# Optimization experiments

Hardware: AMD Instinct MI355X
Metric: run time of the kernel (lower is better)

## Reference

```python
import jax, jax.numpy as jnp
import numpy as np
from jax import lax

RADIUS = 0.3
NSAMPLE = 16
NPROP = 256
NHB = 12
NSC = 18
NCLS = 18
BNEPS = 1e-5


def setup_inputs() -> dict:
    key = jax.random.key(0)
    ks = jax.random.split(key, 10)
    B, K, C = 32, 2048, 256
    OUT = 2 + 3 + NHB * 2 + NSC * 4 + NCLS  # 119
    return {
        "xyz": jax.random.uniform(ks[0], (B, K, 3), jnp.float32),
        "features": jax.random.normal(ks[1], (B, C, K), jnp.float32),
        "sa_w1": jax.random.normal(ks[2], (256, C + 3), jnp.float32) * 0.05,
        "sa_w2": jax.random.normal(ks[3], (256, 256), jnp.float32) * 0.05,
        "sa_w3": jax.random.normal(ks[4], (256, 256), jnp.float32) * 0.05,
        "sa_gamma": jnp.ones((3, 256), jnp.float32),
        "sa_beta": jnp.zeros((3, 256), jnp.float32),
        "sa_mean": jnp.zeros((3, 256), jnp.float32),
        "sa_var": jnp.ones((3, 256), jnp.float32),
        "p_w1": jax.random.normal(ks[5], (256, 256), jnp.float32) * 0.05,
        "p_w2": jax.random.normal(ks[6], (256, 256), jnp.float32) * 0.05,
        "p_w3": jax.random.normal(ks[7], (OUT, 256), jnp.float32) * 0.05,
        "p_b3": jnp.zeros((OUT,), jnp.float32),
        "p_gamma": jnp.ones((2, 256), jnp.float32),
        "p_beta": jnp.zeros((2, 256), jnp.float32),
        "p_mean": jnp.zeros((2, 256), jnp.float32),
        "p_var": jnp.ones((2, 256), jnp.float32),
        "mean_size_arr": jax.random.uniform(ks[8], (NSC, 3), jnp.float32, 0.3, 1.5),
    }


def fps(xyz, npoint):
    # iterative furthest point sampling, starts at index 0 (matches CUDA kernel)
    B, K, _ = xyz.shape

    def body(carry, _):
        dist, far = carry
        centroid = jnp.take_along_axis(xyz, far[:, None, None], axis=1)  # (B,1,3)
        d = jnp.sum((xyz - centroid) ** 2, axis=-1)  # (B,K)
        dist = jnp.minimum(dist, d)
        nxt = jnp.argmax(dist, axis=-1).astype(jnp.int32)
        return (dist, nxt), far

    init = (jnp.full((B, K), 1e10, xyz.dtype), jnp.zeros((B,), jnp.int32))
    _, inds = lax.scan(body, init, None, length=npoint)
    return jnp.transpose(inds, (1, 0))  # (B, npoint)


def ball_query(new_xyz, xyz):
    # first NSAMPLE points (in original index order) within RADIUS; pad with first hit
    B, K, _ = xyz.shape
    d2 = jnp.sum((new_xyz[:, :, None, :] - xyz[:, None, :, :]) ** 2, axis=-1)  # (B,P,K)
    within = d2 < RADIUS * RADIUS
    cand = jnp.where(within, jnp.arange(K, dtype=jnp.int32)[None, None, :], K)
    cand = jnp.sort(cand, axis=-1)[..., :NSAMPLE]
    first = cand[..., :1]  # query point itself is always within radius
    return jnp.where(cand == K, first, cand)  # (B,P,NSAMPLE)


def box_corners(center_unnorm, size, angle):
    # flip_axis_to_camera: X right, Y down (-z_up), Z forward (y_up)
    cc = jnp.stack([center_unnorm[..., 0], center_unnorm[..., 2], -center_unnorm[..., 1]], axis=-1)
    c, s = jnp.cos(angle), jnp.sin(angle)
    zz, oo = jnp.zeros_like(angle), jnp.ones_like(angle)
    R = jnp.stack([c, zz, s, zz, oo, zz, -s, zz, c], axis=-1).reshape(angle.shape + (3, 3))
    sx = jnp.asarray([1, 1, -1, -1, 1, 1, -1, -1], jnp.float32)
    sy = jnp.asarray([1, 1, 1, 1, -1, -1, -1, -1], jnp.float32)
    sz = jnp.asarray([1, -1, -1, 1, 1, -1, -1, 1], jnp.float32)
    xc = size[..., 0:1] * sx * 0.5
    yc = size[..., 2:3] * sy * 0.5
    zc = size[..., 1:2] * sz * 0.5
    corners = jnp.stack([xc, yc, zc], axis=-2)  # (B,P,3,8)
    out = jnp.einsum('bpij,bpjk->bpik', R, corners) + cc[..., None]
    return jnp.transpose(out, (0, 1, 3, 2))  # (B,P,8,3)


def _forward(xyz, features, sa_w1, sa_w2, sa_w3, sa_gamma, sa_beta, sa_mean, sa_var,
             p_w1, p_w2, p_w3, p_b3, p_gamma, p_beta, p_mean, p_var, mean_size_arr):
    B, K, _ = xyz.shape
    inds = fps(xyz, NPROP)  # (B,P) vote_fps
    new_xyz = jnp.take_along_axis(xyz, inds[..., None], axis=1)  # (B,P,3)
    idx = ball_query(new_xyz, xyz)  # (B,P,S)
    flat = idx.reshape(B, -1)
    g_xyz = jnp.take_along_axis(xyz, flat[..., None], axis=1).reshape(B, NPROP, NSAMPLE, 3)
    g_xyz = (g_xyz - new_xyz[:, :, None, :]) / RADIUS  # normalize_xyz
    g_feat = jnp.take_along_axis(features, flat[:, None, :], axis=2).reshape(B, -1, NPROP, NSAMPLE)
    x = jnp.concatenate([jnp.transpose(g_xyz, (0, 3, 1, 2)), g_feat], axis=1)  # (B,3+C,P,S)
    for i, w in enumerate((sa_w1, sa_w2, sa_w3)):
        x = jnp.einsum('oc,bcps->bops', w, x)
        scale = (sa_gamma[i] / jnp.sqrt(sa_var[i] + BNEPS))[None, :, None, None]
        x = jax.nn.relu((x - sa_mean[i][None, :, None, None]) * scale + sa_beta[i][None, :, None, None])
    y = jnp.max(x, axis=-1)  # (B,256,P) max-pool over neighbors
    for i, w in enumerate((p_w1, p_w2)):
        y = jnp.einsum('oc,bcp->bop', w, y)
        scale = (p_gamma[i] / jnp.sqrt(p_var[i] + BNEPS))[None, :, None]
        y = jax.nn.relu((y - p_mean[i][None, :, None]) * scale + p_beta[i][None, :, None])
    net = jnp.einsum('oc,bcp->bop', p_w3, y) + p_b3[None, :, None]
    nt = jnp.transpose(net, (0, 2, 1))  # (B,P,119)
    obj = nt[..., 0:2]
    center = new_xyz + nt[..., 2:5]
    o = 5 + NHB * 2
    size_scores = nt[..., o:o + NSC]
    srn = nt[..., o + NSC:o + NSC * 4].reshape(B, NPROP, NSC, 3)
    sem = nt[..., o + NSC * 4:]
    size_res = srn * mean_size_arr[None, None]
    best = jnp.argmax(size_scores, axis=-1)
    pred_size = jnp.take_along_axis(size_res + mean_size_arr[None, None],
                                    best[..., None, None], axis=2)[:, :, 0, :]
    corners = box_corners(center, pred_size, jnp.zeros_like(center[..., 0]))
    sem_logits = jnp.concatenate(
        [sem, jnp.argmin(obj, axis=-1, keepdims=True).astype(nt.dtype) * 1e10], axis=-1)
    obj_prob = jax.nn.softmax(obj, axis=-1)[..., 1]
    sem_prob = jax.nn.softmax(sem, axis=-1)
    return obj, center, size_scores, size_res, pred_size, sem, corners, sem_logits, obj_prob, sem_prob


def reference(xyz, features, sa_w1, sa_w2, sa_w3, sa_gamma, sa_beta, sa_mean, sa_var,
              p_w1, p_w2, p_w3, p_b3, p_gamma, p_beta, p_mean, p_var, mean_size_arr):
    return _forward(xyz, features, sa_w1, sa_w2, sa_w3, sa_gamma, sa_beta, sa_mean, sa_var,
                    p_w1, p_w2, p_w3, p_b3, p_gamma, p_beta, p_mean, p_var, mean_size_arr)
```

## Files before the change

kernel.cpp:

```cpp
#include <hip/hip_runtime.h>
#include <math.h>

#define B_   32
#define K_   2048
#define C_   256
#define P_   256
#define S_   16
#define OUTC 119

#define OFF0 0
#define OFF1 16384
#define OFF2 40960
#define OFF3 188416
#define OFF4 630784
#define OFF5 655360
#define OFF6 802816
#define OFF7 999424
#define OFF8 1155072
#define OFF9 1163264

typedef _Float16 half8  __attribute__((ext_vector_type(8)));
typedef _Float16 half4h __attribute__((ext_vector_type(4)));
typedef float    f32x4  __attribute__((ext_vector_type(4)));
#define MFMA16 __builtin_amdgcn_mfma_f32_16x16x32_f16

#define XT 65

__device__ __forceinline__ float sqdist_rn(float ax, float ay, float az,
                                           float bx, float by, float bz) {
  float dx = __fsub_rn(ax, bx), dy = __fsub_rn(ay, by), dz = __fsub_rn(az, bz);
  return __fadd_rn(__fadd_rn(__fmul_rn(dx, dx), __fmul_rn(dy, dy)),
                   __fmul_rn(dz, dz));
}

__device__ __forceinline__ unsigned umax_(unsigned a, unsigned b) {
  return a > b ? a : b;
}
__device__ __forceinline__ unsigned umin_(unsigned a, unsigned b) {
  return a < b ? a : b;
}
__device__ __forceinline__ unsigned wave_red_umax(unsigned x) {
  x = umax_(x, (unsigned)__builtin_amdgcn_update_dpp(0, (int)x, 0x111, 0xf, 0xf, false));
  x = umax_(x, (unsigned)__builtin_amdgcn_update_dpp(0, (int)x, 0x112, 0xf, 0xf, false));
  x = umax_(x, (unsigned)__builtin_amdgcn_update_dpp(0, (int)x, 0x114, 0xf, 0xf, false));
  x = umax_(x, (unsigned)__builtin_amdgcn_update_dpp(0, (int)x, 0x118, 0xf, 0xf, false));
  x = umax_(x, (unsigned)__builtin_amdgcn_update_dpp(0, (int)x, 0x142, 0xf, 0xf, false));
  x = umax_(x, (unsigned)__builtin_amdgcn_update_dpp(0, (int)x, 0x143, 0xf, 0xf, false));
  return x;
}
__device__ __forceinline__ unsigned wave_red_umin(unsigned x) {
  x = umin_(x, (unsigned)__builtin_amdgcn_update_dpp(-1, (int)x, 0x111, 0xf, 0xf, false));
  x = umin_(x, (unsigned)__builtin_amdgcn_update_dpp(-1, (int)x, 0x112, 0xf, 0xf, false));
  x = umin_(x, (unsigned)__builtin_amdgcn_update_dpp(-1, (int)x, 0x114, 0xf, 0xf, false));
  x = umin_(x, (unsigned)__builtin_amdgcn_update_dpp(-1, (int)x, 0x118, 0xf, 0xf, false));
  x = umin_(x, (unsigned)__builtin_amdgcn_update_dpp(-1, (int)x, 0x142, 0xf, 0xf, false));
  x = umin_(x, (unsigned)__builtin_amdgcn_update_dpp(-1, (int)x, 0x143, 0xf, 0xf, false));
  return x;
}

__device__ __forceinline__ void wsplit_body(
    int r, int t, const float* __restrict__ w1, const float* __restrict__ w2,
    const float* __restrict__ w3, const float* __restrict__ pw1,
    const float* __restrict__ pw2, const float* __restrict__ gma,
    const float* __restrict__ var, const float* __restrict__ pg,
    const float* __restrict__ pv, _Float16* __restrict__ w1h,
    _Float16* __restrict__ w1l, _Float16* __restrict__ w2h,
    _Float16* __restrict__ w2l, _Float16* __restrict__ w3h,
    _Float16* __restrict__ w3l, _Float16* __restrict__ p1h,
    _Float16* __restrict__ p1l, _Float16* __restrict__ p2h,
    _Float16* __restrict__ p2l, float* __restrict__ bns) {
  if (r == 656) {
    for (int u = t; u < 768; u += 64) bns[u] = gma[u] / sqrtf(var[u] + 1e-5f);
    for (int u = t; u < 512; u += 64)
      bns[768 + u] = pg[u] / sqrtf(pv[u] + 1e-5f);
    return;
  }
  const float* src;
  _Float16 *dh, *dl;
  int ot, ks, nks, K, remap = 0;
  if (r < 144) {
    src = w1; dh = w1h; dl = w1l; ot = r / 9; ks = r % 9; nks = 9; K = 259;
    remap = 1;
  } else if (r < 272) {
    const int rr = r - 144;
    src = w2; dh = w2h; dl = w2l; ot = rr >> 3; ks = rr & 7; nks = 8; K = 256;
  } else if (r < 400) {
    const int rr = r - 272;
    src = w3; dh = w3h; dl = w3l; ot = rr >> 3; ks = rr & 7; nks = 8; K = 256;
  } else if (r < 528) {
    const int rr = r - 400;
    src = pw1; dh = p1h; dl = p1l; ot = rr >> 3; ks = rr & 7; nks = 8; K = 256;
  } else {
    const int rr = r - 528;
    src = pw2; dh = p2h; dl = p2l; ot = rr >> 3; ks = rr & 7; nks = 8; K = 256;
  }
  const int m = t & 15, q = t >> 4;
  const float* row = src + (ot * 16 + m) * K;
  half8 vh, vl;
#pragma unroll
  for (int j = 0; j < 8; j++) {
    const int c = ks * 32 + q * 8 + j;
    float v;
    if (remap) {
      v = (c < 3) ? row[c] : (c >= 8 && c < 264) ? row[c - 5] : 0.f;
    } else {
      v = (c < K) ? row[c] : 0.f;
    }
    const _Float16 hi = (_Float16)v;
    vh[j] = hi;
    vl[j] = (_Float16)(v - (float)hi);
  }
  const int base = ((ot * nks + ks) * 64 + t) * 8;
  *(half8*)&dh[base] = vh;
  *(half8*)&dl[base] = vl;
}

__global__ __launch_bounds__(256) void fused_pre_kernel(
    const float* __restrict__ xyz, float* __restrict__ new_xyz,
    const float* __restrict__ features, _Float16* __restrict__ ftH,
    _Float16* __restrict__ ftL,
    const float* __restrict__ w1, const float* __restrict__ w2,
    const float* __restrict__ w3, const float* __restrict__ pw1,
    const float* __restrict__ pw2, const float* __restrict__ gma,
    const float* __restrict__ var, const float* __restrict__ pg,
    const float* __restrict__ pv, _Float16* __restrict__ w1h,
    _Float16* __restrict__ w1l, _Float16* __restrict__ w2h,
    _Float16* __restrict__ w2l, _Float16* __restrict__ w3h,
    _Float16* __restrict__ w3l, _Float16* __restrict__ p1h,
    _Float16* __restrict__ p1l, _Float16* __restrict__ p2h,
    _Float16* __restrict__ p2l, float* __restrict__ bns) {
  __shared__ __align__(16) char smem_pre[32768];
  __shared__ uint2 redw[2][4];
  const int bid = blockIdx.x;

  if (bid >= 197) {
    const int idx = bid - 197;
    const int b = idx >> 7, rem = idx & 127;
    const int c0 = (rem >> 5) * 64, k0 = (rem & 31) * 64;
    float* tl = (float*)smem_pre;
    const int w = threadIdx.x >> 6, lane = threadIdx.x & 63;
    const float* fb = features + (size_t)b * C_ * K_;
#pragma unroll
    for (int r = 0; r < 16; r++) {
      const int cl = r * 4 + w;
      tl[cl * 65 + lane] = fb[(size_t)(c0 + cl) * K_ + k0 + lane];
    }
    __syncthreads();
#pragma unroll
    for (int r = 0; r < 16; r++) {
      const int kl = r * 4 + w;
      const float v = tl[lane * 65 + kl];
      const _Float16 hi = (_Float16)v;
      const size_t o = ((size_t)b * K_ + k0 + kl) * C_ + c0 + lane;
      ftH[o] = hi;
      ftL[o] = (_Float16)(v - (float)hi);
    }
    return;
  }

  if (bid >= 32) {
    const int sub = (bid - 32) * 4 + (threadIdx.x >> 6);
    if (sub < 657)
      wsplit_body(sub, threadIdx.x & 63, w1, w2, w3, pw1, pw2, gma, var, pg,
                  pv, w1h, w1l, w2h, w2l, w3h, w3l, p1h, p1l, p2h, p2l, bns);
    return;
  }

  const int b = bid, t = threadIdx.x;
  const int lane = t & 63, w = t >> 6;
  float4* pts = (float4*)smem_pre;
  const float* xb = xyz + b * K_ * 3;
  float px[8], py[8], pz[8], dist[8];
#pragma unroll
  for (int j = 0; j < 8; j++) {
    const int k = t + 256 * j;
    const float x = xb[3 * k + 0];
    const float yv = xb[3 * k + 1];
    const float z = xb[3 * k + 2];
    px[j] = x; py[j] = yv; pz[j] = z;
    dist[j] = 1e10f;
    pts[k] = make_float4(x, yv, z, 0.f);
  }
  __syncthreads();
  int far = 0;
  for (int i = 0; i < P_; i++) {
    const float4 c = pts[far];
    if (t == 0) {
      float* nx = new_xyz + (b * P_ + i) * 3;
      nx[0] = c.x; nx[1] = c.y; nx[2] = c.z;
    }
    float bv = -1.f;
    int bj = 0;
#pragma unroll
    for (int j = 0; j < 8; j++) {
      const float d = sqdist_rn(px[j], py[j], pz[j], c.x, c.y, c.z);
      dist[j] = fminf(dist[j], d);
      if (dist[j] > bv) { bv = dist[j]; bj = j; }
    }
    const unsigned bvb = __float_as_uint(bv);
    const unsigned gw = wave_red_umax(bvb);
    const unsigned gmaxw = (unsigned)__builtin_amdgcn_readlane((int)gw, 63);
    const unsigned kg = (unsigned)(bj * 256 + t);
    const unsigned key2 = (bvb == gmaxw) ? kg : 0xFFFFFFFFu;
    const unsigned kw = wave_red_umin(key2);
    if (lane == 63) redw[i & 1][w] = make_uint2(gmaxw, kw);
    __syncthreads();
    const uint2 r0 = redw[i & 1][0], r1 = redw[i & 1][1];
    const uint2 r2 = redw[i & 1][2], r3 = redw[i & 1][3];
    const unsigned g = umax_(umax_(r0.x, r1.x), umax_(r2.x, r3.x));
    unsigned fk = 0xFFFFFFFFu;
    if (r0.x == g) fk = umin_(fk, r0.y);
    if (r1.x == g) fk = umin_(fk, r1.y);
    if (r2.x == g) fk = umin_(fk, r2.y);
    if (r3.x == g) fk = umin_(fk, r3.y);
    far = (int)fk;
  }
}

__global__ __launch_bounds__(1024) void ballq_kernel(
    const float* __restrict__ xyz, const float* __restrict__ new_xyz,
    int* __restrict__ idxw) {
  const int blk = blockIdx.x;
  const int b = blk >> 4, pg = (blk & 15) * 16, t = threadIdx.x;
  __shared__ __align__(16) float4 pts[K_];
  const float* xb = xyz + b * K_ * 3;
#pragma unroll
  for (int j = 0; j < 2; j++) {
    const int k = t + 1024 * j;
    pts[k] = make_float4(xb[3 * k + 0], xb[3 * k + 1], xb[3 * k + 2], 0.f);
  }
  __syncthreads();
  const float r2 = (float)(0.3 * 0.3);
  const int w = t >> 6, lane = t & 63;
  const int p = pg + w;
  const float nx = new_xyz[(b * P_ + p) * 3 + 0];
  const float ny = new_xyz[(b * P_ + p) * 3 + 1];
  const float nz = new_xyz[(b * P_ + p) * 3 + 2];
  int* ob = idxw + (b * P_ + p) * S_;
  unsigned msk = 0u;
#pragma unroll
  for (int j = 0; j < 32; j++) {
    const float4 q = pts[j * 64 + lane];
    const float d2 = sqdist_rn(q.x, q.y, q.z, nx, ny, nz);
    msk |= (d2 < r2 ? 1u : 0u) << j;
  }
  int cnt = 0, first = -1;
  for (int j = 0; j < 32; j++) {
    const unsigned long long bal = __ballot((msk >> j) & 1u);
    if (bal != 0ull && first < 0) first = j * 64 + (__ffsll(bal) - 1);
    const int c = (int)__popcll(bal);
    if ((msk >> j) & 1u) {
      const int pos = cnt + (int)__popcll(bal & ((1ull << lane) - 1ull));
      if (pos < S_) ob[pos] = j * 64 + lane;
    }
    cnt += c;
    if (cnt >= S_) break;
  }
  if (cnt < S_ && lane < S_ - cnt) ob[cnt + lane] = first;
}

__global__ __launch_bounds__(512, 4) void sa_kernel(
    const float* __restrict__ xyz, const float* __restrict__ features,
    const _Float16* __restrict__ ftH, const _Float16* __restrict__ ftL,
    const int use_ft,
    const _Float16* __restrict__ w1h, const _Float16* __restrict__ w1l,
    const _Float16* __restrict__ w2h, const _Float16* __restrict__ w2l,
    const _Float16* __restrict__ w3h, const _Float16* __restrict__ w3l,
    const float* __restrict__ bns, const float* __restrict__ mu,
    const float* __restrict__ bta, const float* __restrict__ new_xyz,
    const int* __restrict__ idxw, float* __restrict__ y) {
  const int blk = blockIdx.x;
  const int b = blk >> 6, p0 = (blk & 63) * 4, t = threadIdx.x;
  __shared__ __align__(16) _Float16 Xh[36 * XT * 8];
  __shared__ __align__(16) _Float16 Xl[36 * XT * 8];
  __shared__ __align__(16) float red[4 * 256];
  __shared__ int k_sh[64];

  if (t < 64) k_sh[t] = idxw[(b * P_ + p0) * S_ + t];
  if (t < 192) {
    const int tile = 32 + t / 48, row = 16 + (t % 48);
    const half8 z8 = {};
    *(half8*)&Xh[(tile * XT + row) * 8] = z8;
    *(half8*)&Xl[(tile * XT + row) * 8] = z8;
  }
  __syncthreads();
  if (t < 64) {
    const int st = t >> 4, m = t & 15, k = k_sh[t];
    const float* xb = xyz + b * K_ * 3;
    const float* nx = new_xyz + (b * P_ + p0 + st) * 3;
    const int base = (st * XT + m) * 8;
#pragma unroll
    for (int c = 0; c < 3; c++) {
      const float v = (xb[3 * k + c] - nx[c]) / 0.3f;
      const _Float16 hi = (_Float16)v;
      Xh[base + c] = hi;
      Xl[base + c] = (_Float16)(v - (float)hi);
    }
#pragma unroll
    for (int j = 3; j < 8; j++) {
      Xh[base + j] = (_Float16)0.f;
      Xl[base + j] = (_Float16)0.f;
    }
  }
  if (use_ft) {
    for (int u = t; u < 2048; u += 512) {
      const int s = u >> 5, ch = u & 31;
      const int c = 8 + ch * 8;
      const int ks = c >> 5, q2 = (c >> 3) & 3;
      const int st = s >> 4, m = s & 15;
      const size_t ro = ((size_t)b * K_ + k_sh[s]) * C_ + ch * 8;
      const int row = (q2 * 16 + m) ^ (ks & 7);
      const int dst = ((ks * 4 + st) * XT + row) * 8;
      *(half8*)&Xh[dst] = *(const half8*)&ftH[ro];
      *(half8*)&Xl[dst] = *(const half8*)&ftL[ro];
    }
  } else {
    const int cl = t & 255, hf = t >> 8;
    const float* fb = features + (size_t)b * C_ * K_ + (size_t)cl * K_;
    const int c = 8 + cl;
    const int ks = c >> 5, q2 = (c >> 3) & 3, j = c & 7;
    const int s0 = hf * 32;
#pragma unroll 8
    for (int s = s0; s < s0 + 32; s++) {
      const float v = fb[k_sh[s]];
      const _Float16 hi = (_Float16)v;
      const int row = (q2 * 16 + (s & 15)) ^ (ks & 7);
      const int dst = ((ks * 4 + (s >> 4)) * XT + row) * 8 + j;
      Xh[dst] = hi;
      Xl[dst] = (_Float16)(v - (float)hi);
    }
  }

  const int lane = t & 63, w = t >> 6;
  const int m = lane & 15, q = lane >> 4;

  f32x4 acc[2][4];
  half8 rAh[2][2], rAl[2][2];
#pragma unroll
  for (int i = 0; i < 2; i++) {
    rAh[0][i] = *(const half8*)&w1h[(((2 * w + i) * 9 + 0) * 64 + lane) * 8];
    rAl[0][i] = *(const half8*)&w1l[(((2 * w + i) * 9 + 0) * 64 + lane) * 8];
    rAh[1][i] = *(const half8*)&w1h[(((2 * w + i) * 9 + 1) * 64 + lane) * 8];
    rAl[1][i] = *(const half8*)&w1l[(((2 * w + i) * 9 + 1) * 64 + lane) * 8];
  }
  __syncthreads();

#pragma unroll
  for (int l = 0; l < 3; l++) {
    const int nks = (l == 0) ? 9 : 8;
    const int base = (l == 0) ? 0 : (l == 1) ? 9 : 17;
#pragma unroll
    for (int i = 0; i < 2; i++)
#pragma unroll
      for (int s = 0; s < 4; s++) acc[i][s] = (f32x4){0.f, 0.f, 0.f, 0.f};
#pragma unroll
    for (int ks = 0; ks < nks; ks++) {
      const int par = (base + ks) & 1;
      half8 Ah[2], Al[2];
#pragma unroll
      for (int i = 0; i < 2; i++) { Ah[i] = rAh[par][i]; Al[i] = rAl[par][i]; }
      {
        int ln = l, kn = ks + 2;
        if (kn >= nks) { kn -= nks; ln = l + 1; }
        if (ln < 3) {
          const _Float16* Ph = (ln == 0) ? w1h : (ln == 1) ? w2h : w3h;
          const _Float16* Pl = (ln == 0) ? w1l : (ln == 1) ? w2l : w3l;
          const int nk2 = (ln == 0) ? 9 : 8;
#pragma unroll
          for (int i = 0; i < 2; i++) {
            const int off = (((2 * w + i) * nk2 + kn) * 64 + lane) * 8;
            rAh[par][i] = *(const half8*)&Ph[off];
            rAl[par][i] = *(const half8*)&Pl[off];
          }
        }
      }
      const int rsw = lane ^ (ks & 7);
#pragma unroll
      for (int s = 0; s < 4; s++) {
        const int tb = ((ks * 4 + s) * XT + rsw) * 8;
        const half8 Bh = *(const half8*)&Xh[tb];
        const half8 Bl = *(const half8*)&Xl[tb];
#pragma unroll
        for (int i = 0; i < 2; i++) {
          acc[i][s] = MFMA16(Ah[i], Bh, acc[i][s], 0, 0, 0);
          acc[i][s] = MFMA16(Ah[i], Bl, acc[i][s], 0, 0, 0);
          acc[i][s] = MFMA16(Al[i], Bh, acc[i][s], 0, 0, 0);
        }
      }
    }

    if (l < 2) {
      __syncthreads();
#pragma unroll
      for (int i = 0; i < 2; i++) {
        const int c0 = (2 * w + i) * 16 + q * 4;
        const int ks2 = c0 >> 5, q2 = (c0 >> 3) & 3, j0 = c0 & 7;
        const f32x4 sc4 = *(const f32x4*)&bns[l * 256 + c0];
        const f32x4 m4 = *(const f32x4*)&mu[l * 256 + c0];
        const f32x4 b4 = *(const f32x4*)&bta[l * 256 + c0];
        const int row = (q2 * 16 + m) ^ (ks2 & 7);
#pragma unroll
        for (int s = 0; s < 4; s++) {
          half4h vh, vl;
#pragma unroll
          for (int r = 0; r < 4; r++) {
            const float v = fmaxf((acc[i][s][r] - m4[r]) * sc4[r] + b4[r], 0.f);
            const _Float16 hi = (_Float16)v;
            vh[r] = hi;
            vl[r] = (_Float16)(v - (float)hi);
          }
          const int dst = ((ks2 * 4 + s) * XT + row) * 8 + j0;
          *(half4h*)&Xh[dst] = vh;
          *(half4h*)&Xl[dst] = vl;
        }
      }
      __syncthreads();
    } else {
#pragma unroll
      for (int i = 0; i < 2; i++)
#pragma unroll
        for (int s = 0; s < 4; s++)
#pragma unroll
          for (int r = 0; r < 4; r++) {
            float v = acc[i][s][r];
            v = fmaxf(v, __shfl_xor(v, 1));
            v = fmaxf(v, __shfl_xor(v, 2));
            v = fmaxf(v, __shfl_xor(v, 4));
            v = fmaxf(v, __shfl_xor(v, 8));
            acc[i][s][r] = v;
          }
      if (m == 0) {
#pragma unroll
        for (int i = 0; i < 2; i++) {
          const int ob = (2 * w + i) * 16 + q * 4;
#pragma unroll
          for (int s = 0; s < 4; s++) *(f32x4*)&red[s * 256 + ob] = acc[i][s];
        }
      }
      __syncthreads();
      for (int u = t; u < 1024; u += 512) {
        const int pl = u >> 8, col = u & 255;
        const float sc2 = bns[512 + col];
        const float mu2 = mu[512 + col], bt2 = bta[512 + col];
        const float raw = red[pl * 256 + col];
        y[(b * P_ + p0 + pl) * 256 + col] = fmaxf((raw - mu2) * sc2 + bt2, 0.f);
      }
    }
  }
}

__global__ __launch_bounds__(256, 2) void phead_kernel(
    const float* __restrict__ y, const _Float16* __restrict__ p1h,
    const _Float16* __restrict__ p1l, const _Float16* __restrict__ p2h,
    const _Float16* __restrict__ p2l, const float* __restrict__ pw3,
    const float* __restrict__ pb3, const float* __restrict__ bns,
    const float* __restrict__ pm, const float* __restrict__ pb,
    const float* __restrict__ new_xyz, const float* __restrict__ msa,
    float* __restrict__ out) {
  const int blk = blockIdx.x;
  const int b = blk >> 4, p0 = (blk & 15) * 16, t = threadIdx.x;
  __shared__ __align__(16) char smem[58624];
  _Float16* X0h = (_Float16*)smem;
  _Float16* X0l = (_Float16*)(smem + 8448);
  _Float16* Hh  = (_Float16*)(smem + 16896);
  _Float16* Hl  = (_Float16*)(smem + 25344);
  float*    Wt  = (float*)smem;
  float*    Y2  = (float*)(smem + 33792);
  float*    net_s = (float*)(smem + 50432);

  {
#pragma unroll 4
    for (int s = 0; s < 16; s++) {
      const float v = y[(size_t)(b * P_ + p0 + s) * C_ + t];
      const _Float16 hi = (_Float16)v;
      X0h[s * 264 + t] = hi;
      X0l[s * 264 + t] = (_Float16)(v - (float)hi);
    }
  }
  const int lane = t & 63, w = t >> 6;
  const int m = lane & 15, q = lane >> 4;

  f32x4 acc[4];
  half8 pAh[4], pAl[4];
#pragma unroll
  for (int i = 0; i < 4; i++) {
    const int off = (((4 * w + i) * 8) * 64 + lane) * 8;
    pAh[i] = *(const half8*)&p1h[off];
    pAl[i] = *(const half8*)&p1l[off];
  }
  __syncthreads();

#pragma unroll
  for (int l = 0; l < 2; l++) {
    const _Float16* Xih = l ? Hh : X0h;
    const _Float16* Xil = l ? Hl : X0l;
#pragma unroll
    for (int i = 0; i < 4; i++) acc[i] = (f32x4){0.f, 0.f, 0.f, 0.f};
    for (int ks = 0; ks < 8; ks++) {
      half8 Ah[4], Al[4];
#pragma unroll
      for (int i = 0; i < 4; i++) { Ah[i] = pAh[i]; Al[i] = pAl[i]; }
      {
        int ln = l, kn = ks + 1;
        if (kn == 8) { ln = l + 1; kn = 0; }
        if (ln < 2) {
          const _Float16* Ph = ln ? p2h : p1h;
          const _Float16* Pl = ln ? p2l : p1l;
#pragma unroll
          for (int i = 0; i < 4; i++) {
            const int off = (((4 * w + i) * 8 + kn) * 64 + lane) * 8;
            pAh[i] = *(const half8*)&Ph[off];
            pAl[i] = *(const half8*)&Pl[off];
          }
        }
      }
      const int xo = ks * 32 + q * 8;
      const half8 Bh = *(const half8*)&Xih[m * 264 + xo];
      const half8 Bl = *(const half8*)&Xil[m * 264 + xo];
#pragma unroll
      for (int i = 0; i < 4; i++) {
        acc[i] = MFMA16(Ah[i], Bh, acc[i], 0, 0, 0);
        acc[i] = MFMA16(Ah[i], Bl, acc[i], 0, 0, 0);
        acc[i] = MFMA16(Al[i], Bh, acc[i], 0, 0, 0);
      }
    }
#pragma unroll
    for (int i = 0; i < 4; i++) {
      const int ob = (4 * w + i) * 16 + q * 4;
      const f32x4 sc4 = *(const f32x4*)&bns[768 + l * 256 + ob];
      const f32x4 m4 = *(const f32x4*)&pm[l * 256 + ob];
      const f32x4 b4 = *(const f32x4*)&pb[l * 256 + ob];
      if (l == 0) {
        half4h vh, vl;
#pragma unroll
        for (int r = 0; r < 4; r++) {
          const float v = fmaxf((acc[i][r] - m4[r]) * sc4[r] + b4[r], 0.f);
          const _Float16 hi = (_Float16)v;
          vh[r] = hi;
          vl[r] = (_Float16)(v - (float)hi);
        }
        *(half4h*)&Hh[m * 264 + ob] = vh;
        *(half4h*)&Hl[m * 264 + ob] = vl;
      } else {
        f32x4 r4;
#pragma unroll
        for (int r = 0; r < 4; r++)
          r4[r] = fmaxf((acc[i][r] - m4[r]) * sc4[r] + b4[r], 0.f);
        *(f32x4*)&Y2[m * 260 + ob] = r4;
      }
    }
    __syncthreads();
  }

  {
    const int o = t & 127, ph = t >> 7;
    float a3[8];
#pragma unroll
    for (int pp = 0; pp < 8; pp++) a3[pp] = 0.f;
    for (int tile = 0; tile < 16; tile++) {
      const int c0 = tile * 16;
      for (int u = t; u < 119 * 4; u += 256) {
        int oo = u >> 2, qq = u & 3;
        *(float4*)&Wt[(qq * 128 + oo) * 4] =
            *(const float4*)(pw3 + oo * 256 + c0 + qq * 4);
      }
      __syncthreads();
      if (o < 119) {
#pragma unroll
        for (int j4 = 0; j4 < 4; j4++) {
          const float4 wv = *(const float4*)&Wt[(j4 * 128 + o) * 4];
#pragma unroll
          for (int pp = 0; pp < 8; pp++) {
            const float4 xv =
                *(const float4*)&Y2[(ph * 8 + pp) * 260 + c0 + j4 * 4];
            a3[pp] = fmaf(wv.x, xv.x, a3[pp]);
            a3[pp] = fmaf(wv.y, xv.y, a3[pp]);
            a3[pp] = fmaf(wv.z, xv.z, a3[pp]);
            a3[pp] = fmaf(wv.w, xv.w, a3[pp]);
          }
        }
      }
      __syncthreads();
    }
    if (o < 119) {
      const float bb = pb3[o];
#pragma unroll
      for (int pp = 0; pp < 8; pp++)
        net_s[(ph * 8 + pp) * 120 + o] = a3[pp] + bb;
    }
  }
  __syncthreads();

  if (t < 16) {
    const int gi = b * P_ + p0 + t;
    const float* nr = &net_s[t * 120];
    const float nx = new_xyz[gi * 3 + 0];
    const float ny = new_xyz[gi * 3 + 1];
    const float nz = new_xyz[gi * 3 + 2];
    const float obj0 = nr[0], obj1 = nr[1];
    out[OFF0 + gi * 2 + 0] = obj0;
    out[OFF0 + gi * 2 + 1] = obj1;
    const float cx = nx + nr[2], cy = ny + nr[3], cz = nz + nr[4];
    out[OFF1 + gi * 3 + 0] = cx;
    out[OFF1 + gi * 3 + 1] = cy;
    out[OFF1 + gi * 3 + 2] = cz;
    float bv = -1e30f;
    int bi = 0;
#pragma unroll
    for (int i = 0; i < 18; i++) {
      float v = nr[29 + i];
      out[OFF2 + gi * 18 + i] = v;
      if (v > bv) { bv = v; bi = i; }
    }
#pragma unroll
    for (int i = 0; i < 18; i++)
#pragma unroll
      for (int j = 0; j < 3; j++)
        out[OFF3 + gi * 54 + i * 3 + j] =
            __fmul_rn(nr[47 + i * 3 + j], msa[i * 3 + j]);
    float ps[3];
#pragma unroll
    for (int j = 0; j < 3; j++) {
      ps[j] = __fadd_rn(__fmul_rn(nr[47 + bi * 3 + j], msa[bi * 3 + j]),
                        msa[bi * 3 + j]);
      out[OFF4 + gi * 3 + j] = ps[j];
    }
    float sm = -1e30f;
#pragma unroll
    for (int i = 0; i < 18; i++) {
      float v = nr[101 + i];
      out[OFF5 + gi * 18 + i] = v;
      out[OFF7 + gi * 19 + i] = v;
      sm = fmaxf(sm, v);
    }
    out[OFF7 + gi * 19 + 18] = (obj0 <= obj1) ? 0.f : 1e10f;
    const float cc0 = cx, cc1 = cz, cc2 = -cy;
    const float sxk[8] = {1, 1, -1, -1, 1, 1, -1, -1};
    const float syk[8] = {1, 1, 1, 1, -1, -1, -1, -1};
    const float szk[8] = {1, -1, -1, 1, 1, -1, -1, 1};
#pragma unroll
    for (int k = 0; k < 8; k++) {
      out[OFF6 + gi * 24 + 3 * k + 0] = cc0 + ps[0] * sxk[k] * 0.5f;
      out[OFF6 + gi * 24 + 3 * k + 1] = cc1 + ps[2] * syk[k] * 0.5f;
      out[OFF6 + gi * 24 + 3 * k + 2] = cc2 + ps[1] * szk[k] * 0.5f;
    }
    {
      const float m2 = fmaxf(obj0, obj1);
      const float e0 = expf(obj0 - m2), e1 = expf(obj1 - m2);
      out[OFF8 + gi] = e1 / (e0 + e1);
    }
    {
      float ev[18], es = 0.f;
#pragma unroll
      for (int i = 0; i < 18; i++) {
        ev[i] = expf(nr[101 + i] - sm);
        es += ev[i];
      }
#pragma unroll
      for (int i = 0; i < 18; i++) out[OFF9 + gi * 18 + i] = ev[i] / es;
    }
  }
}

extern "C" void kernel_launch(void* const* d_in, const int* in_sizes, int n_in,
                              void* d_out, int out_size, void* d_ws,
                              size_t ws_size, hipStream_t stream) {
  (void)in_sizes; (void)n_in; (void)out_size;
  const float* xyz      = (const float*)d_in[0];
  const float* features = (const float*)d_in[1];
  const float* w1       = (const float*)d_in[2];
  const float* w2       = (const float*)d_in[3];
  const float* w3       = (const float*)d_in[4];
  const float* gma      = (const float*)d_in[5];
  const float* bta      = (const float*)d_in[6];
  const float* mu       = (const float*)d_in[7];
  const float* var      = (const float*)d_in[8];
  const float* pw1      = (const float*)d_in[9];
  const float* pw2      = (const float*)d_in[10];
  const float* pw3      = (const float*)d_in[11];
  const float* pb3      = (const float*)d_in[12];
  const float* pg       = (const float*)d_in[13];
  const float* pb       = (const float*)d_in[14];
  const float* pm       = (const float*)d_in[15];
  const float* pv       = (const float*)d_in[16];
  const float* msa      = (const float*)d_in[17];
  float* out = (float*)d_out;

  char* ws = (char*)d_ws;
  float*     new_xyz = (float*)ws;
  int*       idxw    = (int*)(ws + 98304);
  float*     yb      = (float*)(ws + 622592);
  _Float16*  w1h     = (_Float16*)(ws + 9011200);
  _Float16*  w1l     = (_Float16*)(ws + 9158656);
  _Float16*  w2h     = (_Float16*)(ws + 9306112);
  _Float16*  w2l     = (_Float16*)(ws + 9437184);
  _Float16*  w3h     = (_Float16*)(ws + 9568256);
  _Float16*  w3l     = (_Float16*)(ws + 9699328);
  float*     bns     = (float*)(ws + 9830400);
  _Float16*  p1h     = (_Float16*)(ws + 9835520);
  _Float16*  p1l     = (_Float16*)(ws + 9966592);
  _Float16*  p2h     = (_Float16*)(ws + 10097664);
  _Float16*  p2l     = (_Float16*)(ws + 10228736);
  _Float16*  ftH     = (_Float16*)(ws + 10359808);
  _Float16*  ftL     = (_Float16*)(ws + 43914240);

  const int use_ft = (ws_size >= 77468672ull) ? 1 : 0;
  const int npre = use_ft ? (197 + 4096) : 197;

  fused_pre_kernel<<<npre, 256, 0, stream>>>(xyz, new_xyz, features, ftH, ftL,
                                             w1, w2, w3, pw1, pw2, gma, var,
                                             pg, pv, w1h, w1l, w2h, w2l, w3h,
                                             w3l, p1h, p1l, p2h, p2l, bns);
  ballq_kernel<<<B_ * 16, 1024, 0, stream>>>(xyz, new_xyz, idxw);
  sa_kernel<<<B_ * 64, 512, 0, stream>>>(xyz, features, ftH, ftL, use_ft,
                                         w1h, w1l, w2h, w2l, w3h, w3l, bns,
                                         mu, bta, new_xyz, idxw, yb);
  phead_kernel<<<B_ * 16, 256, 0, stream>>>(yb, p1h, p1l, p2h, p2l, pw3, pb3,
                                            bns, pm, pb, new_xyz, msa, out);
}
```

Measured before the change: 432.1 us.

## Pack FPS argmax into 64-bit key and retile SA MLP warps

FPS now uses packed float2 distance math and merges the max value and smallest index into one 64-bit key, so each step needs a single DPP reduction instead of two. The SA MLP kernel changes how warps split the work: each warp now owns 4 output-channel tiles × 2 sample tiles instead of 2×4, and weight prefetch goes one k-step ahead instead of two. The intent is to shorten the serial FPS critical path and to reuse B-operand loads across more MFMAs. The trade-off is more A-fragment registers per warp and a shorter prefetch distance, which could hurt latency hiding.

New measurement: 455.5 us. 1.05x slower.

```diff
diff --git a/kernel.cpp b/kernel.cpp
--- a/kernel.cpp
+++ b/kernel.cpp
@@ -22,6 +22,7 @@
 typedef _Float16 half8  __attribute__((ext_vector_type(8)));
 typedef _Float16 half4h __attribute__((ext_vector_type(4)));
 typedef float    f32x4  __attribute__((ext_vector_type(4)));
+typedef float    f32x2  __attribute__((ext_vector_type(2)));
 #define MFMA16 __builtin_amdgcn_mfma_f32_16x16x32_f16
 
 #define XT 65
@@ -38,24 +39,6 @@
 }
 __device__ __forceinline__ unsigned umin_(unsigned a, unsigned b) {
   return a < b ? a : b;
-}
-__device__ __forceinline__ unsigned wave_red_umax(unsigned x) {
-  x = umax_(x, (unsigned)__builtin_amdgcn_update_dpp(0, (int)x, 0x111, 0xf, 0xf, false));
-  x = umax_(x, (unsigned)__builtin_amdgcn_update_dpp(0, (int)x, 0x112, 0xf, 0xf, false));
-  x = umax_(x, (unsigned)__builtin_amdgcn_update_dpp(0, (int)x, 0x114, 0xf, 0xf, false));
-  x = umax_(x, (unsigned)__builtin_amdgcn_update_dpp(0, (int)x, 0x118, 0xf, 0xf, false));
-  x = umax_(x, (unsigned)__builtin_amdgcn_update_dpp(0, (int)x, 0x142, 0xf, 0xf, false));
-  x = umax_(x, (unsigned)__builtin_amdgcn_update_dpp(0, (int)x, 0x143, 0xf, 0xf, false));
-  return x;
-}
-__device__ __forceinline__ unsigned wave_red_umin(unsigned x) {
-  x = umin_(x, (unsigned)__builtin_amdgcn_update_dpp(-1, (int)x, 0x111, 0xf, 0xf, false));
-  x = umin_(x, (unsigned)__builtin_amdgcn_update_dpp(-1, (int)x, 0x112, 0xf, 0xf, false));
-  x = umin_(x, (unsigned)__builtin_amdgcn_update_dpp(-1, (int)x, 0x114, 0xf, 0xf, false));
-  x = umin_(x, (unsigned)__builtin_amdgcn_update_dpp(-1, (int)x, 0x118, 0xf, 0xf, false));
-  x = umin_(x, (unsigned)__builtin_amdgcn_update_dpp(-1, (int)x, 0x142, 0xf, 0xf, false));
-  x = umin_(x, (unsigned)__builtin_amdgcn_update_dpp(-1, (int)x, 0x143, 0xf, 0xf, false));
-  return x;
 }
 
 __device__ __forceinline__ void wsplit_body(
@@ -130,7 +113,7 @@
     _Float16* __restrict__ p1l, _Float16* __restrict__ p2h,
     _Float16* __restrict__ p2l, float* __restrict__ bns) {
   __shared__ __align__(16) char smem_pre[32768];
-  __shared__ uint2 redw[2][4];
+  __shared__ __align__(16) unsigned long long redk[2][4];
   const int bid = blockIdx.x;
 
   if (bid >= 197) {
@@ -170,15 +153,17 @@
   const int lane = t & 63, w = t >> 6;
   float4* pts = (float4*)smem_pre;
   const float* xb = xyz + b * K_ * 3;
-  float px[8], py[8], pz[8], dist[8];
+  f32x2 px[4], py[4], pz[4], dist[4];
 #pragma unroll
   for (int j = 0; j < 8; j++) {
     const int k = t + 256 * j;
     const float x = xb[3 * k + 0];
     const float yv = xb[3 * k + 1];
     const float z = xb[3 * k + 2];
-    px[j] = x; py[j] = yv; pz[j] = z;
-    dist[j] = 1e10f;
+    px[j >> 1][j & 1] = x;
+    py[j >> 1][j & 1] = yv;
+    pz[j >> 1][j & 1] = z;
+    dist[j >> 1][j & 1] = 1e10f;
     pts[k] = make_float4(x, yv, z, 0.f);
   }
   __syncthreads();
@@ -189,31 +174,49 @@
       float* nx = new_xyz + (b * P_ + i) * 3;
       nx[0] = c.x; nx[1] = c.y; nx[2] = c.z;
     }
-    float bv = -1.f;
-    int bj = 0;
-#pragma unroll
-    for (int j = 0; j < 8; j++) {
-      const float d = sqdist_rn(px[j], py[j], pz[j], c.x, c.y, c.z);
-      dist[j] = fminf(dist[j], d);
-      if (dist[j] > bv) { bv = dist[j]; bj = j; }
-    }
-    const unsigned bvb = __float_as_uint(bv);
-    const unsigned gw = wave_red_umax(bvb);
-    const unsigned gmaxw = (unsigned)__builtin_amdgcn_readlane((int)gw, 63);
-    const unsigned kg = (unsigned)(bj * 256 + t);
-    const unsigned key2 = (bvb == gmaxw) ? kg : 0xFFFFFFFFu;
-    const unsigned kw = wave_red_umin(key2);
-    if (lane == 63) redw[i & 1][w] = make_uint2(gmaxw, kw);
+    {
+#pragma clang fp contract(off)
+      const f32x2 cx = {c.x, c.x}, cy = {c.y, c.y}, cz = {c.z, c.z};
+#pragma unroll
+      for (int j2 = 0; j2 < 4; j2++) {
+        const f32x2 dx = px[j2] - cx;
+        const f32x2 dy = py[j2] - cy;
+        const f32x2 dz = pz[j2] - cz;
+        const f32x2 d = (dx * dx + dy * dy) + dz * dz;
+        dist[j2] = __builtin_elementwise_min(dist[j2], d);
+      }
+    }
+    unsigned long long bkey = 0ull;
+#pragma unroll
+    for (int j2 = 0; j2 < 4; j2++)
+#pragma unroll
+      for (int e = 0; e < 2; e++) {
+        const unsigned kg = (unsigned)((2 * j2 + e) * 256 + t);
+        const unsigned long long key =
+            ((unsigned long long)__float_as_uint(dist[j2][e]) << 32) |
+            (unsigned long long)(0xFFFFFFFFu - kg);
+        bkey = (key > bkey) ? key : bkey;
+      }
+#define RSTEP(ctl)                                                            \
+  {                                                                           \
+    const unsigned olo = (unsigned)__builtin_amdgcn_update_dpp(               \
+        0, (int)(unsigned)bkey, ctl, 0xf, 0xf, false);                        \
+    const unsigned ohi = (unsigned)__builtin_amdgcn_update_dpp(               \
+        0, (int)(unsigned)(bkey >> 32), ctl, 0xf, 0xf, false);                \
+    const unsigned long long o = ((unsigned long long)ohi << 32) | olo;       \
+    bkey = (o > bkey) ? o : bkey;                                             \
+  }
+    RSTEP(0x111) RSTEP(0x112) RSTEP(0x114) RSTEP(0x118)
+    RSTEP(0x142) RSTEP(0x143)
+#undef RSTEP
+    if (lane == 63) redk[i & 1][w] = bkey;
     __syncthreads();
-    const uint2 r0 = redw[i & 1][0], r1 = redw[i & 1][1];
-    const uint2 r2 = redw[i & 1][2], r3 = redw[i & 1][3];
-    const unsigned g = umax_(umax_(r0.x, r1.x), umax_(r2.x, r3.x));
-    unsigned fk = 0xFFFFFFFFu;
-    if (r0.x == g) fk = umin_(fk, r0.y);
-    if (r1.x == g) fk = umin_(fk, r1.y);
-    if (r2.x == g) fk = umin_(fk, r2.y);
-    if (r3.x == g) fk = umin_(fk, r3.y);
-    far = (int)fk;
+    const unsigned long long k0 = redk[i & 1][0], k1 = redk[i & 1][1];
+    const unsigned long long k2 = redk[i & 1][2], k3 = redk[i & 1][3];
+    unsigned long long km = (k0 > k1) ? k0 : k1;
+    km = (k2 > km) ? k2 : km;
+    km = (k3 > km) ? k3 : km;
+    far = (int)(0xFFFFFFFFu - (unsigned)(km & 0xFFFFFFFFull));
   }
 }
 
@@ -333,15 +336,15 @@
 
   const int lane = t & 63, w = t >> 6;
   const int m = lane & 15, q = lane >> 4;
-
-  f32x4 acc[2][4];
-  half8 rAh[2][2], rAl[2][2];
-#pragma unroll
-  for (int i = 0; i < 2; i++) {
-    rAh[0][i] = *(const half8*)&w1h[(((2 * w + i) * 9 + 0) * 64 + lane) * 8];
-    rAl[0][i] = *(const half8*)&w1l[(((2 * w + i) * 9 + 0) * 64 + lane) * 8];
-    rAh[1][i] = *(const half8*)&w1h[(((2 * w + i) * 9 + 1) * 64 + lane) * 8];
-    rAl[1][i] = *(const half8*)&w1l[(((2 * w + i) * 9 + 1) * 64 + lane) * 8];
+  const int og = w & 3, sg = w >> 2;
+
+  f32x4 acc[4][2];
+  half8 rAh[2][4], rAl[2][4];
+#pragma unroll
+  for (int i = 0; i < 4; i++) {
+    const int off = (((og * 4 + i) * 9 + 0) * 64 + lane) * 8;
+    rAh[0][i] = *(const half8*)&w1h[off];
+    rAl[0][i] = *(const half8*)&w1l[off];
   }
   __syncthreads();
 
@@ -350,41 +353,39 @@
     const int nks = (l == 0) ? 9 : 8;
     const int base = (l == 0) ? 0 : (l == 1) ? 9 : 17;
 #pragma unroll
-    for (int i = 0; i < 2; i++)
-#pragma unroll
-      for (int s = 0; s < 4; s++) acc[i][s] = (f32x4){0.f, 0.f, 0.f, 0.f};
+    for (int i = 0; i < 4; i++) {
+      acc[i][0] = (f32x4){0.f, 0.f, 0.f, 0.f};
+      acc[i][1] = (f32x4){0.f, 0.f, 0.f, 0.f};
+    }
 #pragma unroll
     for (int ks = 0; ks < nks; ks++) {
       const int par = (base + ks) & 1;
-      half8 Ah[2], Al[2];
-#pragma unroll
-      for (int i = 0; i < 2; i++) { Ah[i] = rAh[par][i]; Al[i] = rAl[par][i]; }
       {
-        int ln = l, kn = ks + 2;
-        if (kn >= nks) { kn -= nks; ln = l + 1; }
+        int ln = l, kn = ks + 1;
+        if (kn >= nks) { kn = 0; ln = l + 1; }
         if (ln < 3) {
           const _Float16* Ph = (ln == 0) ? w1h : (ln == 1) ? w2h : w3h;
           const _Float16* Pl = (ln == 0) ? w1l : (ln == 1) ? w2l : w3l;
           const int nk2 = (ln == 0) ? 9 : 8;
 #pragma unroll
-          for (int i = 0; i < 2; i++) {
-            const int off = (((2 * w + i) * nk2 + kn) * 64 + lane) * 8;
-            rAh[par][i] = *(const half8*)&Ph[off];
-            rAl[par][i] = *(const half8*)&Pl[off];
+          for (int i = 0; i < 4; i++) {
+            const int off = (((og * 4 + i) * nk2 + kn) * 64 + lane) * 8;
+            rAh[par ^ 1][i] = *(const half8*)&Ph[off];
+            rAl[par ^ 1][i] = *(const half8*)&Pl[off];
           }
         }
       }
       const int rsw = lane ^ (ks & 7);
 #pragma unroll
-      for (int s = 0; s < 4; s++) {
-        const int tb = ((ks * 4 + s) * XT + rsw) * 8;
+      for (int s = 0; s < 2; s++) {
+        const int tb = ((ks * 4 + sg * 2 + s) * XT + rsw) * 8;
         const half8 Bh = *(const half8*)&Xh[tb];
         const half8 Bl = *(const half8*)&Xl[tb];
 #pragma unroll
-        for (int i = 0; i < 2; i++) {
-          acc[i][s] = MFMA16(Ah[i], Bh, acc[i][s], 0, 0, 0);
-          acc[i][s] = MFMA16(Ah[i], Bl, acc[i][s], 0, 0, 0);
-          acc[i][s] = MFMA16(Al[i], Bh, acc[i][s], 0, 0, 0);
+        for (int i = 0; i < 4; i++) {
+          acc[i][s] = MFMA16(rAh[par][i], Bh, acc[i][s], 0, 0, 0);
+          acc[i][s] = MFMA16(rAh[par][i], Bl, acc[i][s], 0, 0, 0);
+          acc[i][s] = MFMA16(rAl[par][i], Bh, acc[i][s], 0, 0, 0);
         }
       }
     }
@@ -392,15 +393,15 @@
     if (l < 2) {
       __syncthreads();
 #pragma unroll
-      for (int i = 0; i < 2; i++) {
-        const int c0 = (2 * w + i) * 16 + q * 4;
+      for (int i = 0; i < 4; i++) {
+        const int c0 = (og * 4 + i) * 16 + q * 4;
         const int ks2 = c0 >> 5, q2 = (c0 >> 3) & 3, j0 = c0 & 7;
         const f32x4 sc4 = *(const f32x4*)&bns[l * 256 + c0];
         const f32x4 m4 = *(const f32x4*)&mu[l * 256 + c0];
         const f32x4 b4 = *(const f32x4*)&bta[l * 256 + c0];
         const int row = (q2 * 16 + m) ^ (ks2 & 7);
 #pragma unroll
-        for (int s = 0; s < 4; s++) {
+        for (int s = 0; s < 2; s++) {
           half4h vh, vl;
 #pragma unroll
           for (int r = 0; r < 4; r++) {
@@ -409,7 +410,7 @@
             vh[r] = hi;
             vl[r] = (_Float16)(v - (float)hi);
           }
-          const int dst = ((ks2 * 4 + s) * XT + row) * 8 + j0;
+          const int dst = ((ks2 * 4 + sg * 2 + s) * XT + row) * 8 + j0;
           *(half4h*)&Xh[dst] = vh;
           *(half4h*)&Xl[dst] = vl;
         }
@@ -417,9 +418,9 @@
       __syncthreads();
     } else {
 #pragma unroll
-      for (int i = 0; i < 2; i++)
-#pragma unroll
-        for (int s = 0; s < 4; s++)
+      for (int i = 0; i < 4; i++)
+#pragma unroll
+        for (int s = 0; s < 2; s++)
 #pragma unroll
           for (int r = 0; r < 4; r++) {
             float v = acc[i][s][r];
@@ -431,10 +432,11 @@
           }
       if (m == 0) {
 #pragma unroll
-        for (int i = 0; i < 2; i++) {
-          const int ob = (2 * w + i) * 16 + q * 4;
-#pragma unroll
-          for (int s = 0; s < 4; s++) *(f32x4*)&red[s * 256 + ob] = acc[i][s];
+        for (int i = 0; i < 4; i++) {
+          const int ob = (og * 4 + i) * 16 + q * 4;
+#pragma unroll
+          for (int s = 0; s < 2; s++)
+            *(f32x4*)&red[(sg * 2 + s) * 256 + ob] = acc[i][s];
         }
       }
       __syncthreads();
```
